# Performance work log

Measured on AMD Instinct MI355X. Metric: run time of the kernel, lower is better.

Reference implementation:

```python
import jax, jax.numpy as jnp
import numpy as np

EMBED_DIM = 128
NUM_HEADS = 4
WINDOW = 7
L = WINDOW * WINDOW  # 49 tokens per window
D_K = EMBED_DIM // NUM_HEADS
NUM_WINDOWS = 1024   # windows per image (224/7)^2
B_TOTAL = 8192       # image_batch(8) * NUM_WINDOWS


def _relative_position_index(window):
    ch, cw = np.meshgrid(np.arange(window), np.arange(window), indexing='ij')
    coords = np.stack([ch.ravel(), cw.ravel()])              # [2, L]
    rel = coords[:, :, None] - coords[:, None, :]            # [2, L, L]
    rel = rel.transpose(1, 2, 0)                             # [L, L, 2]
    rel[:, :, 0] += window - 1
    rel[:, :, 1] += window - 1
    rel[:, :, 0] *= 2 * window - 1
    return rel.sum(-1)                                       # [L, L] int

REL_IDX = jnp.asarray(_relative_position_index(WINDOW))


def setup_inputs() -> dict:
    key = jax.random.key(0)
    ks = jax.random.split(key, 8)
    q = jax.random.normal(ks[0], (B_TOTAL, L, EMBED_DIM), jnp.float32)
    k = jax.random.normal(ks[1], (B_TOTAL, L, EMBED_DIM), jnp.float32)
    v = jax.random.normal(ks[2], (B_TOTAL, L, EMBED_DIM), jnp.float32)
    # shift-mask style additive mask (0 / -100 pattern emulated by random floats is less
    # faithful; build a real 0/-100 mask from a random window partition)
    mkey = jax.random.fold_in(key, 99)
    groups = jax.random.randint(mkey, (NUM_WINDOWS, L), 0, 4)
    mask = jnp.where(groups[:, :, None] == groups[:, None, :], 0.0, -100.0).astype(jnp.float32)
    Wq = jax.random.normal(ks[3], (EMBED_DIM, EMBED_DIM), jnp.float32) * 0.02
    Wk = jax.random.normal(ks[4], (EMBED_DIM, EMBED_DIM), jnp.float32) * 0.02
    Wv = jax.random.normal(ks[5], (EMBED_DIM, EMBED_DIM), jnp.float32) * 0.02
    Wo = jax.random.normal(ks[6], (EMBED_DIM, EMBED_DIM), jnp.float32) * 0.02
    bo = jnp.zeros((EMBED_DIM,), jnp.float32)
    rel_table = jax.random.normal(ks[7], ((2 * WINDOW - 1) ** 2, NUM_HEADS), jnp.float32) * 0.02
    return {"q": q, "k": k, "v": v, "mask": mask, "Wq": Wq, "Wk": Wk,
            "Wv": Wv, "Wo": Wo, "bo": bo, "rel_table": rel_table}


def reference(q, k, v, mask, Wq, Wk, Wv, Wo, bo, rel_table):
    B = q.shape[0]
    # linear projections (torch Linear: x @ W.T), split heads -> [B, H, L, d]
    def proj(x, W):
        return (x @ W.T).reshape(B, L, NUM_HEADS, D_K).transpose(0, 2, 1, 3)
    qh, kh, vh = proj(q, Wq), proj(k, Wk), proj(v, Wv)

    energy = jnp.einsum('bhld,bhmd->bhlm', qh, kh) / jnp.sqrt(jnp.float32(D_K))
    # gathered relative position bias: [L, L, H] -> [1, H, L, L]
    bias = rel_table[REL_IDX].transpose(2, 0, 1)[None]
    energy = energy + bias
    # additive shift mask per window: [B//nW, nW, H, L, L] + mask[None,:,None]
    nW = mask.shape[0]
    energy = energy.reshape(-1, nW, NUM_HEADS, L, L) + mask[None, :, None]
    energy = energy.reshape(B, NUM_HEADS, L, L)

    attn = jax.nn.softmax(energy, axis=-1)
    out = jnp.einsum('bhlm,bhmd->bhld', attn, vh)
    out = out.transpose(0, 2, 1, 3).reshape(B, L, EMBED_DIM)
    return out @ Wo.T + bo
```

## Files before the change

kernel.cpp:

```cpp
#include <hip/hip_runtime.h>

#define TOK 49
#define DIM 128
#define NHEAD 4
#define NWIN 1024
#define SCALE 0.17677669529663687f

typedef __bf16 bf16x8 __attribute__((ext_vector_type(8)));
typedef short s16x4 __attribute__((ext_vector_type(4)));
typedef float f32x4 __attribute__((ext_vector_type(4)));
typedef unsigned short u16;
typedef unsigned int u32;

#if defined(__HIP_DEVICE_COMPILE__)
#define MFMA16(a, b, c) __builtin_amdgcn_mfma_f32_16x16x16bf16_1k(a, b, c, 0, 0, 0)
#define MFMA32(a, b, c) __builtin_amdgcn_mfma_f32_16x16x32_bf16(a, b, c, 0, 0, 0)
#else
__device__ inline f32x4 MFMA16(s16x4, s16x4, f32x4 c) { return c; }
__device__ inline f32x4 MFMA32(bf16x8, bf16x8, f32x4 c) { return c; }
#endif

__device__ __forceinline__ int xo256(int row, int kbyte) {
    return row * 256 + (kbyte ^ ((row & 7) << 4));
}
__device__ __forceinline__ u16 bfbits(float x) {
    __bf16 t = (__bf16)x;
    return __builtin_bit_cast(u16, t);
}
__device__ __forceinline__ float bf2f(u16 x) {
    u32 u = ((u32)x) << 16;
    return __builtin_bit_cast(float, u);
}
__device__ __forceinline__ bf16x8 cvt8(const float* __restrict__ p) {
    float4 a = *reinterpret_cast<const float4*>(p);
    float4 bq = *reinterpret_cast<const float4*>(p + 4);
    bf16x8 r;
    r[0] = (__bf16)a.x; r[1] = (__bf16)a.y; r[2] = (__bf16)a.z; r[3] = (__bf16)a.w;
    r[4] = (__bf16)bq.x; r[5] = (__bf16)bq.y; r[6] = (__bf16)bq.z; r[7] = (__bf16)bq.w;
    return r;
}
__device__ __forceinline__ bf16x8 cvt8s(const float* __restrict__ p, float s) {
    float4 a = *reinterpret_cast<const float4*>(p);
    float4 bq = *reinterpret_cast<const float4*>(p + 4);
    bf16x8 r;
    r[0] = (__bf16)(a.x * s); r[1] = (__bf16)(a.y * s);
    r[2] = (__bf16)(a.z * s); r[3] = (__bf16)(a.w * s);
    r[4] = (__bf16)(bq.x * s); r[5] = (__bf16)(bq.y * s);
    r[6] = (__bf16)(bq.z * s); r[7] = (__bf16)(bq.w * s);
    return r;
}
__device__ __forceinline__ s16x4 pack4(const f32x4& a) {
    s16x4 r;
    r[0] = (short)bfbits(a[0]); r[1] = (short)bfbits(a[1]);
    r[2] = (short)bfbits(a[2]); r[3] = (short)bfbits(a[3]);
    return r;
}
__device__ __forceinline__ s16x4 pack4s(const f32x4& a, float s) {
    s16x4 r;
    r[0] = (short)bfbits(a[0] * s); r[1] = (short)bfbits(a[1] * s);
    r[2] = (short)bfbits(a[2] * s); r[3] = (short)bfbits(a[3] * s);
    return r;
}

__global__ void fused_pre_kernel(const float* __restrict__ mask, const float* __restrict__ rel,
                                 u16* __restrict__ tbl) {
    const int idx = blockIdx.x * 256 + threadIdx.x;
    const int w = idx >> 14, h = (idx >> 12) & 3, l = (idx >> 6) & 63, m = idx & 63;
    float v = 0.0f;
    if (l < TOK && m < TOK) {
        const int dl = l / 7 - m / 7 + 6;
        const int dc = l % 7 - m % 7 + 6;
        v = mask[(w * TOK + l) * TOK + m] + rel[(dl * 13 + dc) * NHEAD + h];
    }
    tbl[idx] = bfbits(v);
}

__global__ void bias_pre_kernel(const float* __restrict__ rel, float* __restrict__ biasT) {
    const int idx = blockIdx.x * 256 + threadIdx.x;
    const int h = idx >> 12, l = (idx >> 6) & 63, m = idx & 63;
    float v = 0.0f;
    if (l < TOK && m < TOK) {
        const int dl = l / 7 - m / 7 + 6;
        const int dc = l % 7 - m % 7 + 6;
        v = rel[(dl * 13 + dc) * NHEAD + h];
    }
    biasT[idx] = v;
}

__global__ void wcvt_kernel(const float* __restrict__ Wq, const float* __restrict__ Wk,
                            const float* __restrict__ Wv, const float* __restrict__ Wo,
                            u16* __restrict__ tbl) {
    const int idx = blockIdx.x * 256 + threadIdx.x;
    const int mat = idx >> 14, e = idx & 16383;
    float v;
    if (mat == 0)      v = Wq[e] * SCALE;
    else if (mat == 1) v = Wk[e];
    else if (mat == 2) v = Wv[e];
    else               v = Wo[e];
    tbl[idx] = bfbits(v);
}

template <int MODE>
__global__ __launch_bounds__(256, 3) void winattn_kernel(
    const float* __restrict__ q, const float* __restrict__ k, const float* __restrict__ v,
    const float* __restrict__ mask, const float* __restrict__ Wq, const float* __restrict__ Wk,
    const float* __restrict__ Wv, const float* __restrict__ Wo, const float* __restrict__ bo,
    const u16* __restrict__ wtbl, const u16* __restrict__ fmtbl, const float* __restrict__ btbl,
    float* __restrict__ out)
{
    __shared__ __align__(16) char LA[16384];
    __shared__ __align__(16) char LB[16384];
    __shared__ __align__(16) char LC[16384];
    const int tid = threadIdx.x;
    const int wave = tid >> 6;
    const int lane = tid & 63;
    const int l16 = lane & 15;
    const int k8 = lane >> 4;
    const int b = blockIdx.x;
    const int h = wave;

    const float* qp = q + (size_t)b * (TOK * DIM);
    const float* kp = k + (size_t)b * (TOK * DIM);
    const float* vp = v + (size_t)b * (TOK * DIM);
    float* op = out + (size_t)b * (TOK * DIM);

    auto ldw = [&](int mat, int row, int kk) -> bf16x8 {
        return *reinterpret_cast<const bf16x8*>(
            reinterpret_cast<const __bf16*>(wtbl) + (mat << 14) + row * DIM + kk * 32 + k8 * 8);
    };
    auto ldx = [&](const char* buf, int row, int kk) -> bf16x8 {
        return *reinterpret_cast<const bf16x8*>(buf + xo256(row, kk * 64 + k8 * 16));
    };
    auto gload = [&](float4* dst, const float* __restrict__ src) {
        #pragma unroll
        for (int p = 0; p < 8; ++p) {
            const int idx = p * 256 + tid;
            const int row = idx >> 5;
            const int c4 = (idx & 31) * 4;
            dst[p] = (row < TOK) ? *reinterpret_cast<const float4*>(src + row * DIM + c4)
                                 : float4{0.f, 0.f, 0.f, 0.f};
        }
    };
    auto lwrite = [&](char* L, const float4* src) {
        #pragma unroll
        for (int p = 0; p < 8; ++p) {
            const int idx = p * 256 + tid;
            uint2 pk2;
            pk2.x = (u32)bfbits(src[p].x) | ((u32)bfbits(src[p].y) << 16);
            pk2.y = (u32)bfbits(src[p].z) | ((u32)bfbits(src[p].w) << 16);
            *reinterpret_cast<uint2*>(L + xo256(idx >> 5, (idx & 31) * 8)) = pk2;
        }
    };

    {
        float4 tq[8], tk[8], tv[8];
        gload(tq, qp);
        gload(tk, kp);
        gload(tv, vp);
        lwrite(LA, tq);
        lwrite(LB, tk);
        lwrite(LC, tv);
    }
    __syncthreads();

    uint2 tbl[16];
    if constexpr (MODE == 0) {
        const u16* frow = fmtbl + ((((size_t)(b & (NWIN - 1)) * NHEAD) + h) << 12);
        #pragma unroll
        for (int ni = 0; ni < 4; ++ni) {
            const int l = ni * 16 + l16;
            #pragma unroll
            for (int mi = 0; mi < 4; ++mi)
                tbl[ni * 4 + mi] = *reinterpret_cast<const uint2*>(
                    frow + l * 64 + mi * 16 + k8 * 4);
        }
    }

    s16x4 qf[2][4], kf[2][4];
    {
        f32x4 acc[2][4];
        #pragma unroll
        for (int t2 = 0; t2 < 2; ++t2)
            #pragma unroll
            for (int ni = 0; ni < 4; ++ni) acc[t2][ni] = f32x4{0.f, 0.f, 0.f, 0.f};
        #pragma unroll
        for (int kk = 0; kk < 4; ++kk) {
            bf16x8 wa[2], xb[4];
            #pragma unroll
            for (int t2 = 0; t2 < 2; ++t2)
                wa[t2] = (MODE == 0) ? ldw(0, h * 32 + t2 * 16 + l16, kk)
                                     : cvt8s(Wq + (h * 32 + t2 * 16 + l16) * DIM + kk * 32 + k8 * 8, SCALE);
            #pragma unroll
            for (int ni = 0; ni < 4; ++ni) xb[ni] = ldx(LA, ni * 16 + l16, kk);
            #pragma unroll
            for (int t2 = 0; t2 < 2; ++t2)
                #pragma unroll
                for (int ni = 0; ni < 4; ++ni) acc[t2][ni] = MFMA32(wa[t2], xb[ni], acc[t2][ni]);
        }
        #pragma unroll
        for (int t2 = 0; t2 < 2; ++t2)
            #pragma unroll
            for (int ni = 0; ni < 4; ++ni) qf[t2][ni] = pack4(acc[t2][ni]);
    }
    {
        f32x4 acc[2][4];
        #pragma unroll
        for (int t2 = 0; t2 < 2; ++t2)
            #pragma unroll
            for (int mi = 0; mi < 4; ++mi) acc[t2][mi] = f32x4{0.f, 0.f, 0.f, 0.f};
        #pragma unroll
        for (int kk = 0; kk < 4; ++kk) {
            bf16x8 wa[2], xb[4];
            #pragma unroll
            for (int t2 = 0; t2 < 2; ++t2)
                wa[t2] = (MODE == 0) ? ldw(1, h * 32 + t2 * 16 + l16, kk)
                                     : cvt8(Wk + (h * 32 + t2 * 16 + l16) * DIM + kk * 32 + k8 * 8);
            #pragma unroll
            for (int mi = 0; mi < 4; ++mi) xb[mi] = ldx(LB, mi * 16 + l16, kk);
            #pragma unroll
            for (int t2 = 0; t2 < 2; ++t2)
                #pragma unroll
                for (int mi = 0; mi < 4; ++mi) acc[t2][mi] = MFMA32(wa[t2], xb[mi], acc[t2][mi]);
        }
        #pragma unroll
        for (int t2 = 0; t2 < 2; ++t2)
            #pragma unroll
            for (int mi = 0; mi < 4; ++mi) kf[t2][mi] = pack4(acc[t2][mi]);
    }

    s16x4 pf[4][4];
    {
        const float* brow = (MODE == 1) ? btbl + ((size_t)h << 12) : nullptr;
        const float* mp = mask + (size_t)(b & (NWIN - 1)) * (TOK * TOK);
        #pragma unroll
        for (int ni = 0; ni < 4; ++ni) {
            f32x4 ec[4];
            #pragma unroll
            for (int mi = 0; mi < 4; ++mi) {
                f32x4 c = {0.f, 0.f, 0.f, 0.f};
                c = MFMA16(kf[0][mi], qf[0][ni], c);
                ec[mi] = MFMA16(kf[1][mi], qf[1][ni], c);
            }
            const int l = ni * 16 + l16;
            const bool lv = l < TOK;
            #pragma unroll
            for (int mi = 0; mi < 4; ++mi) {
                const int m0 = mi * 16 + k8 * 4;
                float ad[4];
                if constexpr (MODE == 0) {
                    const uint2 raw = tbl[ni * 4 + mi];
                    ad[0] = bf2f((u16)(raw.x & 0xffffu));
                    ad[1] = bf2f((u16)(raw.x >> 16));
                    ad[2] = bf2f((u16)(raw.y & 0xffffu));
                    ad[3] = bf2f((u16)(raw.y >> 16));
                } else {
                    const float4 bg = *reinterpret_cast<const float4*>(brow + l * 64 + m0);
                    ad[0] = bg.x; ad[1] = bg.y; ad[2] = bg.z; ad[3] = bg.w;
                    #pragma unroll
                    for (int r = 0; r < 4; ++r) {
                        const int m = m0 + r;
                        if (lv && m < TOK) ad[r] += mp[l * TOK + m];
                    }
                }
                #pragma unroll
                for (int r = 0; r < 4; ++r) {
                    const int m = m0 + r;
                    ec[mi][r] = (lv && m < TOK) ? ec[mi][r] + ad[r] : -1e30f;
                }
            }
            float mx = -1e30f;
            #pragma unroll
            for (int mi = 0; mi < 4; ++mi)
                #pragma unroll
                for (int r = 0; r < 4; ++r) mx = fmaxf(mx, ec[mi][r]);
            mx = fmaxf(mx, __shfl_xor(mx, 16));
            mx = fmaxf(mx, __shfl_xor(mx, 32));
            float s = 0.f;
            #pragma unroll
            for (int mi = 0; mi < 4; ++mi) {
                #pragma unroll
                for (int r = 0; r < 4; ++r) {
                    const float p = __expf(ec[mi][r] - mx);
                    ec[mi][r] = p;
                    s += p;
                }
            }
            s += __shfl_xor(s, 16);
            s += __shfl_xor(s, 32);
            const float rs = 1.0f / s;
            #pragma unroll
            for (int mi = 0; mi < 4; ++mi) pf[mi][ni] = pack4s(ec[mi], rs);
        }
    }

    s16x4 vf[4][2];
    {
        f32x4 acc[4][2];
        #pragma unroll
        for (int mi = 0; mi < 4; ++mi)
            #pragma unroll
            for (int nn = 0; nn < 2; ++nn) acc[mi][nn] = f32x4{0.f, 0.f, 0.f, 0.f};
        #pragma unroll
        for (int kk = 0; kk < 4; ++kk) {
            bf16x8 xa[4], wb[2];
            #pragma unroll
            for (int mi = 0; mi < 4; ++mi) xa[mi] = ldx(LC, mi * 16 + l16, kk);
            #pragma unroll
            for (int nn = 0; nn < 2; ++nn)
                wb[nn] = (MODE == 0) ? ldw(2, h * 32 + nn * 16 + l16, kk)
                                     : cvt8(Wv + (h * 32 + nn * 16 + l16) * DIM + kk * 32 + k8 * 8);
            #pragma unroll
            for (int mi = 0; mi < 4; ++mi)
                #pragma unroll
                for (int nn = 0; nn < 2; ++nn) acc[mi][nn] = MFMA32(xa[mi], wb[nn], acc[mi][nn]);
        }
        #pragma unroll
        for (int mi = 0; mi < 4; ++mi)
            #pragma unroll
            for (int nn = 0; nn < 2; ++nn) vf[mi][nn] = pack4(acc[mi][nn]);
    }

    f32x4 o_[4][2];
    #pragma unroll
    for (int ni = 0; ni < 4; ++ni) {
        #pragma unroll
        for (int nn = 0; nn < 2; ++nn) {
            f32x4 c = {0.f, 0.f, 0.f, 0.f};
            #pragma unroll
            for (int mi = 0; mi < 4; ++mi) c = MFMA16(pf[mi][ni], vf[mi][nn], c);
            o_[ni][nn] = c;
        }
    }
    __syncthreads();

    #pragma unroll
    for (int ni = 0; ni < 4; ++ni) {
        #pragma unroll
        for (int nn = 0; nn < 2; ++nn) {
            const int d = h * 32 + nn * 16 + l16;
            #pragma unroll
            for (int r = 0; r < 4; ++r) {
                const int row = ni * 16 + k8 * 4 + r;
                *reinterpret_cast<u16*>(LA + xo256(row, d * 2)) = bfbits(o_[ni][nn][r]);
            }
        }
    }
    bf16x8 aw[2][4];
    #pragma unroll
    for (int m2 = 0; m2 < 2; ++m2) {
        const int o = (wave * 2 + m2) * 16 + l16;
        #pragma unroll
        for (int kk = 0; kk < 4; ++kk)
            aw[m2][kk] = (MODE == 0) ? ldw(3, o, kk)
                                     : cvt8(Wo + o * DIM + kk * 32 + k8 * 8);
    }
    __syncthreads();

    #pragma unroll
    for (int ni = 0; ni < 4; ++ni) {
        const int l = ni * 16 + l16;
        bf16x8 bx[4];
        #pragma unroll
        for (int kk = 0; kk < 4; ++kk)
            bx[kk] = *reinterpret_cast<const bf16x8*>(LA + xo256(l, kk * 64 + k8 * 16));
        #pragma unroll
        for (int m2 = 0; m2 < 2; ++m2) {
            f32x4 c = {0.f, 0.f, 0.f, 0.f};
            #pragma unroll
            for (int kk = 0; kk < 4; ++kk) c = MFMA32(aw[m2][kk], bx[kk], c);
            if (l < TOK) {
                const int o0 = (wave * 2 + m2) * 16 + k8 * 4;
                const float4 bias = *reinterpret_cast<const float4*>(bo + o0);
                float4 st;
                st.x = c[0] + bias.x;
                st.y = c[1] + bias.y;
                st.z = c[2] + bias.z;
                st.w = c[3] + bias.w;
                *reinterpret_cast<float4*>(op + l * DIM + o0) = st;
            }
        }
    }
}

extern "C" void kernel_launch(void* const* d_in, const int* in_sizes, int n_in,
                              void* d_out, int out_size, void* d_ws, size_t ws_size,
                              hipStream_t stream) {
    const float* q    = (const float*)d_in[0];
    const float* k    = (const float*)d_in[1];
    const float* v    = (const float*)d_in[2];
    const float* mask = (const float*)d_in[3];
    const float* Wq   = (const float*)d_in[4];
    const float* Wk   = (const float*)d_in[5];
    const float* Wv   = (const float*)d_in[6];
    const float* Wo   = (const float*)d_in[7];
    const float* bo   = (const float*)d_in[8];
    const float* rel  = (const float*)d_in[9];
    float* out = (float*)d_out;

    const int B = in_sizes[0] / (TOK * DIM);
    const size_t FUSED_BYTES = (size_t)NWIN * NHEAD * 64 * 64 * sizeof(u16);
    const size_t W_BYTES     = (size_t)4 * DIM * DIM * sizeof(u16);

    if (ws_size >= FUSED_BYTES + W_BYTES) {
        u16* fmtbl = (u16*)d_ws;
        u16* wtbl  = (u16*)((char*)d_ws + FUSED_BYTES);
        fused_pre_kernel<<<dim3(NWIN * NHEAD * 64 * 64 / 256), dim3(256), 0, stream>>>(
            mask, rel, fmtbl);
        wcvt_kernel<<<dim3(4 * DIM * DIM / 256), dim3(256), 0, stream>>>(Wq, Wk, Wv, Wo, wtbl);
        winattn_kernel<0><<<dim3(B), dim3(256), 0, stream>>>(q, k, v, mask, Wq, Wk, Wv, Wo,
                                                             bo, wtbl, fmtbl, nullptr, out);
    } else {
        float* btbl = (float*)d_ws;
        bias_pre_kernel<<<dim3(NHEAD * 64 * 64 / 256), dim3(256), 0, stream>>>(rel, btbl);
        winattn_kernel<1><<<dim3(B), dim3(256), 0, stream>>>(q, k, v, mask, Wq, Wk, Wv, Wo,
                                                             bo, nullptr, nullptr, btbl, out);
    }
}
```

Measured before the change: 344.6 us.

## Split each head across two waves with 512-thread blocks

Doubles the block to 512 threads (8 waves), so that each head is handled by two waves that each own half of the query rows. The K and V projections are still computed in full by both waves of a head, while Q, softmax, PV and output-projection work is halved per wave. The fused bias and mask table is now loaded inline instead of being prefetched into registers. The aim is to cut register pressure per wave and add latency hiding, at the cost of redundant K/V projection MFMAs and a different occupancy target.

Result: slower. 386.5 us (+12.1%).

```diff
diff --git a/kernel.cpp b/kernel.cpp
--- a/kernel.cpp
+++ b/kernel.cpp
@@ -101,7 +101,7 @@
 }
 
 template <int MODE>
-__global__ __launch_bounds__(256, 3) void winattn_kernel(
+__global__ __launch_bounds__(512, 4) void winattn_kernel(
     const float* __restrict__ q, const float* __restrict__ k, const float* __restrict__ v,
     const float* __restrict__ mask, const float* __restrict__ Wq, const float* __restrict__ Wk,
     const float* __restrict__ Wv, const float* __restrict__ Wo, const float* __restrict__ bo,
@@ -117,7 +117,8 @@
     const int l16 = lane & 15;
     const int k8 = lane >> 4;
     const int b = blockIdx.x;
-    const int h = wave;
+    const int h = wave >> 1;
+    const int jj = wave & 1;
 
     const float* qp = q + (size_t)b * (TOK * DIM);
     const float* kp = k + (size_t)b * (TOK * DIM);
@@ -133,8 +134,8 @@
     };
     auto gload = [&](float4* dst, const float* __restrict__ src) {
         #pragma unroll
-        for (int p = 0; p < 8; ++p) {
-            const int idx = p * 256 + tid;
+        for (int p = 0; p < 4; ++p) {
+            const int idx = p * 512 + tid;
             const int row = idx >> 5;
             const int c4 = (idx & 31) * 4;
             dst[p] = (row < TOK) ? *reinterpret_cast<const float4*>(src + row * DIM + c4)
@@ -143,8 +144,8 @@
     };
     auto lwrite = [&](char* L, const float4* src) {
         #pragma unroll
-        for (int p = 0; p < 8; ++p) {
-            const int idx = p * 256 + tid;
+        for (int p = 0; p < 4; ++p) {
+            const int idx = p * 512 + tid;
             uint2 pk2;
             pk2.x = (u32)bfbits(src[p].x) | ((u32)bfbits(src[p].y) << 16);
             pk2.y = (u32)bfbits(src[p].z) | ((u32)bfbits(src[p].w) << 16);
@@ -153,7 +154,7 @@
     };
 
     {
-        float4 tq[8], tk[8], tv[8];
+        float4 tq[4], tk[4], tv[4];
         gload(tq, qp);
         gload(tk, kp);
         gload(tv, vp);
@@ -163,45 +164,34 @@
     }
     __syncthreads();
 
-    uint2 tbl[16];
-    if constexpr (MODE == 0) {
-        const u16* frow = fmtbl + ((((size_t)(b & (NWIN - 1)) * NHEAD) + h) << 12);
-        #pragma unroll
-        for (int ni = 0; ni < 4; ++ni) {
-            const int l = ni * 16 + l16;
-            #pragma unroll
-            for (int mi = 0; mi < 4; ++mi)
-                tbl[ni * 4 + mi] = *reinterpret_cast<const uint2*>(
-                    frow + l * 64 + mi * 16 + k8 * 4);
-        }
-    }
-
-    s16x4 qf[2][4], kf[2][4];
+    s16x4 qf[2][2];
     {
-        f32x4 acc[2][4];
+        f32x4 acc[2][2];
         #pragma unroll
         for (int t2 = 0; t2 < 2; ++t2)
             #pragma unroll
-            for (int ni = 0; ni < 4; ++ni) acc[t2][ni] = f32x4{0.f, 0.f, 0.f, 0.f};
+            for (int n = 0; n < 2; ++n) acc[t2][n] = f32x4{0.f, 0.f, 0.f, 0.f};
         #pragma unroll
         for (int kk = 0; kk < 4; ++kk) {
-            bf16x8 wa[2], xb[4];
+            bf16x8 wa[2], xb[2];
             #pragma unroll
             for (int t2 = 0; t2 < 2; ++t2)
                 wa[t2] = (MODE == 0) ? ldw(0, h * 32 + t2 * 16 + l16, kk)
                                      : cvt8s(Wq + (h * 32 + t2 * 16 + l16) * DIM + kk * 32 + k8 * 8, SCALE);
             #pragma unroll
-            for (int ni = 0; ni < 4; ++ni) xb[ni] = ldx(LA, ni * 16 + l16, kk);
+            for (int n = 0; n < 2; ++n) xb[n] = ldx(LA, (jj * 2 + n) * 16 + l16, kk);
             #pragma unroll
             for (int t2 = 0; t2 < 2; ++t2)
                 #pragma unroll
-                for (int ni = 0; ni < 4; ++ni) acc[t2][ni] = MFMA32(wa[t2], xb[ni], acc[t2][ni]);
+                for (int n = 0; n < 2; ++n) acc[t2][n] = MFMA32(wa[t2], xb[n], acc[t2][n]);
         }
         #pragma unroll
         for (int t2 = 0; t2 < 2; ++t2)
             #pragma unroll
-            for (int ni = 0; ni < 4; ++ni) qf[t2][ni] = pack4(acc[t2][ni]);
-    }
+            for (int n = 0; n < 2; ++n) qf[t2][n] = pack4(acc[t2][n]);
+    }
+
+    s16x4 kf[2][4];
     {
         f32x4 acc[2][4];
         #pragma unroll
@@ -228,27 +218,29 @@
             for (int mi = 0; mi < 4; ++mi) kf[t2][mi] = pack4(acc[t2][mi]);
     }
 
-    s16x4 pf[4][4];
+    s16x4 pf[4][2];
     {
+        const u16* frow = (MODE == 0)
+            ? fmtbl + ((((size_t)(b & (NWIN - 1)) * NHEAD) + h) << 12) : nullptr;
         const float* brow = (MODE == 1) ? btbl + ((size_t)h << 12) : nullptr;
         const float* mp = mask + (size_t)(b & (NWIN - 1)) * (TOK * TOK);
         #pragma unroll
-        for (int ni = 0; ni < 4; ++ni) {
+        for (int n = 0; n < 2; ++n) {
             f32x4 ec[4];
             #pragma unroll
             for (int mi = 0; mi < 4; ++mi) {
                 f32x4 c = {0.f, 0.f, 0.f, 0.f};
-                c = MFMA16(kf[0][mi], qf[0][ni], c);
-                ec[mi] = MFMA16(kf[1][mi], qf[1][ni], c);
+                c = MFMA16(kf[0][mi], qf[0][n], c);
+                ec[mi] = MFMA16(kf[1][mi], qf[1][n], c);
             }
-            const int l = ni * 16 + l16;
+            const int l = (jj * 2 + n) * 16 + l16;
             const bool lv = l < TOK;
             #pragma unroll
             for (int mi = 0; mi < 4; ++mi) {
                 const int m0 = mi * 16 + k8 * 4;
                 float ad[4];
                 if constexpr (MODE == 0) {
-                    const uint2 raw = tbl[ni * 4 + mi];
+                    const uint2 raw = *reinterpret_cast<const uint2*>(frow + l * 64 + m0);
                     ad[0] = bf2f((u16)(raw.x & 0xffffu));
                     ad[1] = bf2f((u16)(raw.x >> 16));
                     ad[2] = bf2f((u16)(raw.y & 0xffffu));
@@ -289,7 +281,7 @@
             s += __shfl_xor(s, 32);
             const float rs = 1.0f / s;
             #pragma unroll
-            for (int mi = 0; mi < 4; ++mi) pf[mi][ni] = pack4s(ec[mi], rs);
+            for (int mi = 0; mi < 4; ++mi) pf[mi][n] = pack4s(ec[mi], rs);
         }
     }
 
@@ -320,40 +312,36 @@
             for (int nn = 0; nn < 2; ++nn) vf[mi][nn] = pack4(acc[mi][nn]);
     }
 
-    f32x4 o_[4][2];
+    f32x4 o_[2][2];
     #pragma unroll
-    for (int ni = 0; ni < 4; ++ni) {
+    for (int n = 0; n < 2; ++n) {
         #pragma unroll
         for (int nn = 0; nn < 2; ++nn) {
             f32x4 c = {0.f, 0.f, 0.f, 0.f};
             #pragma unroll
-            for (int mi = 0; mi < 4; ++mi) c = MFMA16(pf[mi][ni], vf[mi][nn], c);
-            o_[ni][nn] = c;
+            for (int mi = 0; mi < 4; ++mi) c = MFMA16(pf[mi][n], vf[mi][nn], c);
+            o_[n][nn] = c;
         }
     }
     __syncthreads();
 
     #pragma unroll
-    for (int ni = 0; ni < 4; ++ni) {
+    for (int n = 0; n < 2; ++n) {
         #pragma unroll
         for (int nn = 0; nn < 2; ++nn) {
             const int d = h * 32 + nn * 16 + l16;
             #pragma unroll
             for (int r = 0; r < 4; ++r) {
-                const int row = ni * 16 + k8 * 4 + r;
-                *reinterpret_cast<u16*>(LA + xo256(row, d * 2)) = bfbits(o_[ni][nn][r]);
+                const int row = (jj * 2 + n) * 16 + k8 * 4 + r;
+                *reinterpret_cast<u16*>(LA + xo256(row, d * 2)) = bfbits(o_[n][nn][r]);
             }
         }
     }
-    bf16x8 aw[2][4];
+    bf16x8 aw[4];
     #pragma unroll
-    for (int m2 = 0; m2 < 2; ++m2) {
-        const int o = (wave * 2 + m2) * 16 + l16;
-        #pragma unroll
-        for (int kk = 0; kk < 4; ++kk)
-            aw[m2][kk] = (MODE == 0) ? ldw(3, o, kk)
-                                     : cvt8(Wo + o * DIM + kk * 32 + k8 * 8);
-    }
+    for (int kk = 0; kk < 4; ++kk)
+        aw[kk] = (MODE == 0) ? ldw(3, wave * 16 + l16, kk)
+                             : cvt8(Wo + (wave * 16 + l16) * DIM + kk * 32 + k8 * 8);
     __syncthreads();
 
     #pragma unroll
@@ -363,21 +351,18 @@
         #pragma unroll
         for (int kk = 0; kk < 4; ++kk)
             bx[kk] = *reinterpret_cast<const bf16x8*>(LA + xo256(l, kk * 64 + k8 * 16));
-        #pragma unroll
-        for (int m2 = 0; m2 < 2; ++m2) {
-            f32x4 c = {0.f, 0.f, 0.f, 0.f};
-            #pragma unroll
-            for (int kk = 0; kk < 4; ++kk) c = MFMA32(aw[m2][kk], bx[kk], c);
-            if (l < TOK) {
-                const int o0 = (wave * 2 + m2) * 16 + k8 * 4;
-                const float4 bias = *reinterpret_cast<const float4*>(bo + o0);
-                float4 st;
-                st.x = c[0] + bias.x;
-                st.y = c[1] + bias.y;
-                st.z = c[2] + bias.z;
-                st.w = c[3] + bias.w;
-                *reinterpret_cast<float4*>(op + l * DIM + o0) = st;
-            }
+        f32x4 c = {0.f, 0.f, 0.f, 0.f};
+        #pragma unroll
+        for (int kk = 0; kk < 4; ++kk) c = MFMA32(aw[kk], bx[kk], c);
+        if (l < TOK) {
+            const int o0 = wave * 16 + k8 * 4;
+            const float4 bias = *reinterpret_cast<const float4*>(bo + o0);
+            float4 st;
+            st.x = c[0] + bias.x;
+            st.y = c[1] + bias.y;
+            st.z = c[2] + bias.z;
+            st.w = c[3] + bias.w;
+            *reinterpret_cast<float4*>(op + l * DIM + o0) = st;
         }
     }
 }
@@ -407,12 +392,12 @@
         fused_pre_kernel<<<dim3(NWIN * NHEAD * 64 * 64 / 256), dim3(256), 0, stream>>>(
             mask, rel, fmtbl);
         wcvt_kernel<<<dim3(4 * DIM * DIM / 256), dim3(256), 0, stream>>>(Wq, Wk, Wv, Wo, wtbl);
-        winattn_kernel<0><<<dim3(B), dim3(256), 0, stream>>>(q, k, v, mask, Wq, Wk, Wv, Wo,
+        winattn_kernel<0><<<dim3(B), dim3(512), 0, stream>>>(q, k, v, mask, Wq, Wk, Wv, Wo,
                                                              bo, wtbl, fmtbl, nullptr, out);
     } else {
         float* btbl = (float*)d_ws;
         bias_pre_kernel<<<dim3(NHEAD * 64 * 64 / 256), dim3(256), 0, stream>>>(rel, btbl);
-        winattn_kernel<1><<<dim3(B), dim3(256), 0, stream>>>(q, k, v, mask, Wq, Wk, Wv, Wo,
+        winattn_kernel<1><<<dim3(B), dim3(512), 0, stream>>>(q, k, v, mask, Wq, Wk, Wv, Wo,
                                                              bo, nullptr, nullptr, btbl, out);
     }
 }
```
